# Kernel optimization log

Hardware: AMD Instinct MI355X
Metric: run time of the kernel (lower is better)

The kernel has to match this reference:

```python
import jax, jax.numpy as jnp
import numpy as np

NUM_HEADS = 12

def _attn(q, k, v, scale):
    # q,k,v: [..., L, hd]; softmax attention over L (key axis)
    s = jnp.einsum('...qd,...kd->...qk', q, k) * scale
    a = jax.nn.softmax(s, axis=-1)
    return jnp.einsum('...qk,...kd->...qd', a, v)

def setup_inputs() -> dict:
    key = jax.random.key(0)
    k1, k2, k3 = jax.random.split(key, 3)
    B, N, C, D = 8, 256, 16, 768
    x = jax.random.normal(k1, (B, N, C, D), dtype=jnp.float32)
    w_qkv = jax.random.normal(k2, (D, 6 * D), dtype=jnp.float32) * (D ** -0.5)
    w_proj = jax.random.normal(k3, (D, D), dtype=jnp.float32) * (D ** -0.5)
    b_proj = jnp.zeros((D,), dtype=jnp.float32)
    return {"x": x, "w_qkv": w_qkv, "w_proj": w_proj, "b_proj": b_proj}

def reference(x, w_qkv, w_proj, b_proj):
    B, N, C, D = x.shape
    H = NUM_HEADS
    hd = D // H
    scale = hd ** -0.5
    # qkv: [B,N,C,6,H,hd] -> [6,B,H,N,C,hd]
    qkv = (x @ w_qkv).reshape(B, N, C, 6, H, hd).transpose(3, 0, 4, 1, 2, 5)
    qc, kc, qs, ks, vc, vs = qkv[0], qkv[1], qkv[2], qkv[3], qkv[4], qkv[5]
    # spatial attention over N (per channel c): move to [B,H,C,N,hd]
    qs = jnp.swapaxes(qs, -2, -3)
    ks = jnp.swapaxes(ks, -2, -3)
    vs = jnp.swapaxes(vs, -2, -3)
    xs = _attn(qs, ks, vs, scale)          # [B,H,C,N,hd]
    xs = jnp.swapaxes(xs, -2, -3)          # [B,H,N,C,hd]
    # channel attention over C (per token n)
    xc = _attn(qc, kc, vc, scale)          # [B,H,N,C,hd]
    out = xs * xc                           # elementwise combine (fused path)
    # matches torch: x.transpose(1,2).reshape(B,N,C,D)
    out = out.transpose(0, 2, 1, 3, 4).reshape(B, N, C, D)
    return out @ w_proj + b_proj
```

## Files before the change

kernel.cpp:

```cpp
#include <hip/hip_runtime.h>

typedef _Float16 f16;
typedef f16  f16x8 __attribute__((ext_vector_type(8)));
typedef float f32x4 __attribute__((ext_vector_type(4)));

#define S3 3145728LL

__device__ __forceinline__ f32x4 mm(f16x8 a, f16x8 b, f32x4 c) {
  return __builtin_amdgcn_mfma_f32_16x16x32_f16(a, b, c, 0, 0, 0);
}
__device__ __forceinline__ void BAR() { asm volatile("s_barrier" ::: "memory"); }

__device__ __forceinline__ int esw(int t, int col) {
  return t * 128 + ((((col >> 3) ^ ((t ^ (t >> 3)) & 7)) << 3) | (col & 7));
}

__global__ void cvt_T_kernel(const float* __restrict__ in, f16* __restrict__ out,
                             int R, int Cc) {
  __shared__ float tile[32][33];
  int tc = blockIdx.x, tr = blockIdx.y;
  int lr = threadIdx.x & 31, lw = threadIdx.x >> 5;
  int c0 = tc * 32, r0 = tr * 32;
#pragma unroll
  for (int i = 0; i < 4; i++)
    tile[lw + 8 * i][lr] = in[(size_t)(r0 + lw + 8 * i) * Cc + c0 + lr];
  __syncthreads();
#pragma unroll
  for (int i = 0; i < 4; i++)
    out[(size_t)(c0 + lw + 8 * i) * R + r0 + lr] = (f16)tile[lr][lw + 8 * i];
}

__global__ void cvt_x_kernel(const float* __restrict__ in, f16* __restrict__ out) {
  size_t i = ((size_t)blockIdx.x * 256 + threadIdx.x) * 8;
  f32x4 a = __builtin_nontemporal_load((const f32x4*)(in + i));
  f32x4 b = __builtin_nontemporal_load((const f32x4*)(in + i + 4));
  f16x8 o;
#pragma unroll
  for (int j = 0; j < 4; j++) { o[j] = (f16)a[j]; o[4 + j] = (f16)b[j]; }
  *(f16x8*)(out + i) = o;
}

#define QST_A(c, q, kt) __builtin_amdgcn_global_load_lds( \
    (const __attribute__((address_space(1))) void*)(aSrc + (size_t)(q) * 24576 + (size_t)(kt) * 64), \
    (__attribute__((address_space(3))) void*)((char*)lds + (c) * 32768 + (q) * 1024 * 4 + wave * 1024), 16, 0, 0)
#define QST_B(c, q, kt) __builtin_amdgcn_global_load_lds( \
    (const __attribute__((address_space(1))) void*)(bSrc + (size_t)(q) * 24576 + (size_t)(kt) * 64), \
    (__attribute__((address_space(3))) void*)((char*)lds + 16384 + (c) * 32768 + (q) * 1024 * 4 + wave * 1024), 16, 0, 0)

__global__ __launch_bounds__(256, 2) void gemm_qkvT(
    const f16* __restrict__ A, const f16* __restrict__ Bt,
    f16* __restrict__ area, long long cstr_) {
  __shared__ f16 lds[32768];
  size_t cstr = (size_t)cstr_;
  int id  = blockIdx.x;
  int cpx = gridDim.x >> 3;
  int id2 = (id & 7) * cpx + (id >> 3);
  int sr = id2 / 288, rr = id2 % 288;
  int bm = sr * 8 + (rr & 7), bn = rr >> 3;

  int tid = threadIdx.x;
  int wave = tid >> 6, lane = tid & 63;
  int l16 = lane & 15, lq = lane >> 4;
  int wr = wave >> 1, wc = wave & 1;
  int l7 = l16 & 7;
  int cb0 = ((lq) ^ l7) << 4;
  int cb1 = ((4 + lq) ^ l7) << 4;

  const f16* aSrc = A  + (size_t)(bm * 128 + (tid >> 3)) * 768 +
                    (((tid & 7) ^ ((tid >> 3) & 7)) << 3);
  const f16* bSrc = Bt + (size_t)(bn * 128 + (tid >> 3)) * 768 +
                    (((tid & 7) ^ ((tid >> 3) & 7)) << 3);

  f32x4 zz = {0.f, 0.f, 0.f, 0.f};
  f32x4 acc[4][4];
#pragma unroll
  for (int m = 0; m < 4; m++)
#pragma unroll
    for (int n = 0; n < 4; n++) acc[m][n] = zz;

#pragma unroll
  for (int q = 0; q < 4; q++) { QST_A(0, q, 0); }
#pragma unroll
  for (int q = 0; q < 4; q++) { QST_B(0, q, 0); }
#pragma unroll
  for (int q = 0; q < 4; q++) { QST_A(1, q, 1); }
#pragma unroll
  for (int q = 0; q < 4; q++) { QST_B(1, q, 1); }
  asm volatile("s_waitcnt vmcnt(8)" ::: "memory");
  BAR();

  f16x8 af[4][2], bf[4][2];
#pragma unroll 2
  for (int t = 0; t < 12; ++t) {
    int c = t & 1;
    const char* ab = (const char*)lds + c * 32768;
    const char* bb = ab + 16384;
    int rA = wr * 64 + l16;
    int rB = wc * 64 + l16;
#pragma unroll
    for (int mf = 0; mf < 4; mf++) {
      af[mf][0] = *(const f16x8*)(ab + (rA + mf * 16) * 128 + cb0);
      af[mf][1] = *(const f16x8*)(ab + (rA + mf * 16) * 128 + cb1);
    }
#pragma unroll
    for (int nf = 0; nf < 4; nf++) {
      bf[nf][0] = *(const f16x8*)(bb + (rB + nf * 16) * 128 + cb0);
      bf[nf][1] = *(const f16x8*)(bb + (rB + nf * 16) * 128 + cb1);
    }
    asm volatile("s_waitcnt lgkmcnt(0)" ::: "memory");
    BAR();
    if (t < 10) {
#pragma unroll
      for (int q = 0; q < 4; q++) { QST_A(c, q, t + 2); }
#pragma unroll
      for (int q = 0; q < 4; q++) { QST_B(c, q, t + 2); }
    }
    __builtin_amdgcn_s_setprio(1);
#pragma unroll
    for (int ks = 0; ks < 2; ks++)
#pragma unroll
      for (int mf = 0; mf < 4; mf++)
#pragma unroll
        for (int nf = 0; nf < 4; nf++)
          acc[mf][nf] = mm(af[mf][ks], bf[nf][ks], acc[mf][nf]);
    __builtin_amdgcn_s_setprio(0);
    if (t < 10) asm volatile("s_waitcnt vmcnt(8)" ::: "memory");
    else        asm volatile("s_waitcnt vmcnt(0)" ::: "memory");
    BAR();
  }

  int s  = bn / 6;
  int h0 = (bn % 6) * 2;
  size_t comp;
  if (s == 0) comp = 0; else if (s == 1) comp = 1; else if (s == 2) comp = 3;
  else if (s == 3) comp = 4; else if (s == 4) comp = 2; else comp = 5;
  int g = (bm * 128) >> 12;
  size_t base = comp * cstr + (size_t)g * S3;
  int n0 = (bm & 31) * 8;

  __syncthreads();
#pragma unroll
  for (int mi = 0; mi < 4; mi++)
#pragma unroll
    for (int ni = 0; ni < 4; ni++)
#pragma unroll
      for (int r = 0; r < 4; r++) {
        int t = wr * 64 + mi * 16 + lq * 4 + r;
        int col = wc * 64 + ni * 16 + l16;
        lds[esw(t, col)] = (f16)acc[mi][ni][r];
      }
  __syncthreads();

  if (s < 2) {
#pragma unroll
    for (int i = 0; i < 4; i++) {
      int u = wave * 4 + i;
      int hl = u >> 3, j16 = u & 7;
#pragma unroll
      for (int half = 0; half < 2; half++) {
        int e0 = half * 512 + lane * 8;
        int cc = e0 >> 6, d0 = e0 & 63;
        f16x8 v = *(const f16x8*)&lds[esw(j16 * 16 + cc, hl * 64 + d0)];
        __builtin_nontemporal_store(v, (f16x8*)&area[base +
            (size_t)(h0 + hl) * 262144 + (size_t)(n0 + j16) * 1024 + e0]);
      }
    }
  } else if (s < 4) {
#pragma unroll
    for (int i = 0; i < 8; i++) {
      int u = wave * 8 + i;
      int hl = u >> 4, cc = u & 15;
      int e = lane * 8;
      int nl = e >> 6, d0 = e & 63;
      f16x8 v = *(const f16x8*)&lds[esw(nl * 16 + cc, hl * 64 + d0)];
      __builtin_nontemporal_store(v, (f16x8*)&area[base +
          (size_t)((h0 + hl) * 16 + cc) * 16384 + (size_t)n0 * 64 + e]);
    }
  } else if (s == 4) {
#pragma unroll
    for (int i = 0; i < 4; i++) {
      int u = wave * 4 + i;
      int hl = u >> 3, j8 = u & 7;
#pragma unroll
      for (int half = 0; half < 2; half++) {
        int e0 = half * 512 + lane * 8;
        int d0 = e0 >> 4, cb = e0 & 15;
        f16x8 v;
#pragma unroll
        for (int j = 0; j < 8; j++)
          v[j] = lds[esw(j8 * 16 + cb + j, hl * 64 + d0)];
        __builtin_nontemporal_store(v, (f16x8*)&area[base +
            (size_t)((h0 + hl) * 256 + n0 + j8) * 1024 + e0]);
      }
    }
  } else {
#pragma unroll
    for (int i = 0; i < 8; i++) {
      int u = wave * 8 + i;
      int hl = u >> 4, cc = u & 15;
      int e = lane * 8;
      int d0 = e >> 3;
      f16x8 v;
#pragma unroll
      for (int j = 0; j < 8; j++)
        v[j] = lds[esw(j * 16 + cc, hl * 64 + d0)];
      __builtin_nontemporal_store(v, (f16x8*)&area[base +
          ((size_t)((h0 + hl) * 16 + cc) * 32 + (bm & 31)) * 512 + e]);
    }
  }
}

#define STG_A(c, q, kt) __builtin_amdgcn_global_load_lds( \
    (const __attribute__((address_space(1))) void*)(aSrc + (size_t)(q) * 49152 + (size_t)(kt) * 64), \
    (__attribute__((address_space(3))) void*)(lds + (c) * 32768 + (q) * 4096 + wave * 512), 16, 0, 0)
#define STG_B(c, q, kt) __builtin_amdgcn_global_load_lds( \
    (const __attribute__((address_space(1))) void*)(bSrc + (size_t)(q) * 49152 + (size_t)(kt) * 64), \
    (__attribute__((address_space(3))) void*)(lds + 16384 + (c) * 32768 + (q) * 4096 + wave * 512), 16, 0, 0)

__global__ __launch_bounds__(512, 2) void gemm_proj8(
    const f16* __restrict__ A, const f16* __restrict__ Bt,
    const float* __restrict__ bias, float* __restrict__ Cout) {
  __shared__ f16 lds[65536];
  int id  = blockIdx.x;
  int cpx = gridDim.x >> 3;
  int id2 = (id & 7) * cpx + (id >> 3);
  int sr = id2 / 24, rr = id2 % 24;
  int bm = sr * 8 + (rr & 7), bn = rr >> 3;

  int tid = threadIdx.x;
  int wave = tid >> 6, lane = tid & 63;
  int l16 = lane & 15, lq = lane >> 4;
  int wr = wave >> 2, wc = wave & 3;
  int sx  = (l16 & 7) << 4;
  int cb0 = (lq * 16) ^ sx;
  int cb1 = (64 + lq * 16) ^ sx;

  int scol = ((tid & 7) ^ ((tid >> 3) & 7)) << 3;
  const f16* aSrc = A  + (size_t)(bm * 256 + (tid >> 3)) * 768 + scol;
  const f16* bSrc = Bt + (size_t)(bn * 256 + (tid >> 3)) * 768 + scol;

  f32x4 zz = {0.f, 0.f, 0.f, 0.f};
  f32x4 acc[8][4];
#pragma unroll
  for (int m = 0; m < 8; m++)
#pragma unroll
    for (int n = 0; n < 4; n++) acc[m][n] = zz;

  STG_A(0, 0, 0); STG_A(0, 1, 0); STG_A(0, 2, 0); STG_A(0, 3, 0);
  STG_B(0, 0, 0); STG_B(0, 1, 0); STG_B(0, 2, 0); STG_B(0, 3, 0);
  STG_A(1, 1, 1); STG_A(1, 3, 1);
  STG_B(1, 0, 1); STG_B(1, 1, 1);
  asm volatile("s_waitcnt vmcnt(4)" ::: "memory");
  BAR();

  f16x8 af[4][2], ag[4][2], bf[2][2], bg[2][2];
#pragma unroll 2
  for (int t = 0; t < 12; ++t) {
    int c = t & 1, nb = c ^ 1;
    const char* ab = (const char*)lds + c * 65536;
    const char* bb = ab + 32768;
    int rA = wr * 128 + l16;
    int rB = wc * 64 + l16;
#pragma unroll
    for (int mf = 0; mf < 4; mf++) {
      af[mf][0] = *(const f16x8*)(ab + (rA + mf * 16) * 128 + cb0);
      af[mf][1] = *(const f16x8*)(ab + (rA + mf * 16) * 128 + cb1);
    }
#pragma unroll
    for (int nf = 0; nf < 2; nf++) {
      bf[nf][0] = *(const f16x8*)(bb + (rB + nf * 16) * 128 + cb0);
      bf[nf][1] = *(const f16x8*)(bb + (rB + nf * 16) * 128 + cb1);
      bg[nf][0] = *(const f16x8*)(bb + (rB + 32 + nf * 16) * 128 + cb0);
      bg[nf][1] = *(const f16x8*)(bb + (rB + 32 + nf * 16) * 128 + cb1);
    }
    if (t < 11) {
      STG_B(nb, 2, t + 1); STG_B(nb, 3, t + 1);
      STG_A(nb, 0, t + 1); STG_A(nb, 2, t + 1);
    }
    BAR();
    __builtin_amdgcn_s_setprio(1);
#pragma unroll
    for (int ks = 0; ks < 2; ks++)
#pragma unroll
      for (int mf = 0; mf < 4; mf++)
#pragma unroll
        for (int nf = 0; nf < 2; nf++) {
          acc[mf][nf]     = mm(af[mf][ks], bf[nf][ks], acc[mf][nf]);
          acc[mf][2 + nf] = mm(af[mf][ks], bg[nf][ks], acc[mf][2 + nf]);
        }
    __builtin_amdgcn_s_setprio(0);
    BAR();
#pragma unroll
    for (int mf = 0; mf < 4; mf++) {
      ag[mf][0] = *(const f16x8*)(ab + (rA + 64 + mf * 16) * 128 + cb0);
      ag[mf][1] = *(const f16x8*)(ab + (rA + 64 + mf * 16) * 128 + cb1);
    }
    if (t < 10) {
      STG_A(c, 1, t + 2); STG_A(c, 3, t + 2);
      STG_B(c, 0, t + 2); STG_B(c, 1, t + 2);
    }
    BAR();
    __builtin_amdgcn_s_setprio(1);
#pragma unroll
    for (int ks = 0; ks < 2; ks++)
#pragma unroll
      for (int mf = 0; mf < 4; mf++)
#pragma unroll
        for (int nf = 0; nf < 2; nf++) {
          acc[4 + mf][nf]     = mm(ag[mf][ks], bf[nf][ks], acc[4 + mf][nf]);
          acc[4 + mf][2 + nf] = mm(ag[mf][ks], bg[nf][ks], acc[4 + mf][2 + nf]);
        }
    __builtin_amdgcn_s_setprio(0);
    if (t < 10) asm volatile("s_waitcnt vmcnt(4)" ::: "memory");
    else        asm volatile("s_waitcnt vmcnt(0)" ::: "memory");
    BAR();
  }

#pragma unroll
  for (int ni = 0; ni < 4; ni++) {
    int col = bn * 256 + wc * 64 + ni * 16 + l16;
    float bb = bias[col];
#pragma unroll
    for (int mi = 0; mi < 8; mi++) {
#pragma unroll
      for (int r = 0; r < 4; r++) {
        int row = bm * 256 + wr * 128 + (mi >> 2) * 64 + (mi & 3) * 16 + lq * 4 + r;
        __builtin_nontemporal_store(acc[mi][ni][r] + bb,
                                    &Cout[(size_t)row * 768 + col]);
      }
    }
  }
}

__global__ __launch_bounds__(512) void attn_spat_kernel(f16* __restrict__ area,
                                                        long long cstr_) {
  size_t cstr = (size_t)cstr_;
  int blk = blockIdx.x;
  int g = blk / 192, rem = blk % 192;
  int h = rem >> 4, c = rem & 15;
  size_t goff = (size_t)g * S3;
  const f16* qs = area + 3 * cstr + goff + (size_t)((h * 16 + c) * 256) * 64;
  const f16* ks = area + 4 * cstr + goff + (size_t)((h * 16 + c) * 256) * 64;
  const f16* vsb = area + 5 * cstr + goff + (size_t)(h * 16 + c) * 16384;
  f16* xs = area + 6 * cstr + goff + (size_t)((h * 16 + c) * 256) * 64;

  int wave = threadIdx.x >> 6, lane = threadIdx.x & 63;
  int l16 = lane & 15, lq = lane >> 4;
  __shared__ f16 plds[8][32][40];

  f32x4 zz = {0.f, 0.f, 0.f, 0.f};
  f16x8 aq[2][2];
#pragma unroll
  for (int m = 0; m < 2; m++)
#pragma unroll
    for (int kd = 0; kd < 2; kd++)
      aq[m][kd] = *(const f16x8*)&qs[(size_t)(wave * 32 + m * 16 + l16) * 64 + kd * 32 + lq * 8];

  f32x4 o[2][4];
  float mrow[2][4], lrow[2][4];
#pragma unroll
  for (int m = 0; m < 2; m++) {
#pragma unroll
    for (int n = 0; n < 4; n++) o[m][n] = zz;
#pragma unroll
    for (int r = 0; r < 4; r++) { mrow[m][r] = -1e30f; lrow[m][r] = 0.f; }
  }

  for (int kc = 0; kc < 8; kc++) {
    int k0 = kc * 32;
    f16x8 bk00 = *(const f16x8*)&ks[(size_t)(k0 + l16) * 64 + lq * 8];
    f16x8 bk01 = *(const f16x8*)&ks[(size_t)(k0 + l16) * 64 + 32 + lq * 8];
    f16x8 bk10 = *(const f16x8*)&ks[(size_t)(k0 + 16 + l16) * 64 + lq * 8];
    f16x8 bk11 = *(const f16x8*)&ks[(size_t)(k0 + 16 + l16) * 64 + 32 + lq * 8];
    f32x4 st[2][2];
#pragma unroll
    for (int m = 0; m < 2; m++) {
      st[m][0] = mm(aq[m][1], bk01, mm(aq[m][0], bk00, zz));
      st[m][1] = mm(aq[m][1], bk11, mm(aq[m][0], bk10, zz));
    }
#pragma unroll
    for (int m = 0; m < 2; m++) {
#pragma unroll
      for (int r = 0; r < 4; r++) {
        float s0 = st[m][0][r] * 0.125f, s1 = st[m][1][r] * 0.125f;
        float t = fmaxf(s0, s1);
        t = fmaxf(t, __shfl_xor(t, 1));
        t = fmaxf(t, __shfl_xor(t, 2));
        t = fmaxf(t, __shfl_xor(t, 4));
        t = fmaxf(t, __shfl_xor(t, 8));
        float mold = mrow[m][r];
        float mnew = fmaxf(mold, t);
        float fac  = __expf(mold - mnew);
        mrow[m][r] = mnew;
        float p0 = __expf(s0 - mnew), p1 = __expf(s1 - mnew);
        lrow[m][r] = lrow[m][r] * fac + p0 + p1;
        o[m][0][r] *= fac; o[m][1][r] *= fac; o[m][2][r] *= fac; o[m][3][r] *= fac;
        int prow = m * 16 + lq * 4 + r;
        plds[wave][prow][l16]      = (f16)p0;
        plds[wave][prow][16 + l16] = (f16)p1;
      }
    }
    f16x8 ap0 = *(const f16x8*)&plds[wave][l16][lq * 8];
    f16x8 ap1 = *(const f16x8*)&plds[wave][16 + l16][lq * 8];
#pragma unroll
    for (int n = 0; n < 4; n++) {
      f16x8 bv = *(const f16x8*)&vsb[((k0 >> 3) + lq) * 512 + (n * 16 + l16) * 8];
      o[0][n] = mm(ap0, bv, o[0][n]);
      o[1][n] = mm(ap1, bv, o[1][n]);
    }
  }
#pragma unroll
  for (int m = 0; m < 2; m++)
#pragma unroll
    for (int r = 0; r < 4; r++) {
      float l = lrow[m][r];
      l += __shfl_xor(l, 1);
      l += __shfl_xor(l, 2);
      l += __shfl_xor(l, 4);
      l += __shfl_xor(l, 8);
      lrow[m][r] = 1.0f / l;
    }
#pragma unroll
  for (int m = 0; m < 2; m++)
#pragma unroll
    for (int n = 0; n < 4; n++)
#pragma unroll
      for (int r = 0; r < 4; r++) {
        int row = wave * 32 + m * 16 + lq * 4 + r;
        xs[(size_t)row * 64 + n * 16 + l16] = (f16)(o[m][n][r] * lrow[m][r]);
      }
}

__global__ __launch_bounds__(256) void attn_chan_kernel(f16* __restrict__ area,
                                                        long long cstr_) {
  size_t cstr = (size_t)cstr_;
  int blk = blockIdx.x;
  int g = blk >> 8, n = blk & 255;
  size_t goff = (size_t)g * S3;
  int wave = threadIdx.x >> 6, lane = threadIdx.x & 63;
  int l16 = lane & 15, lq = lane >> 4;
  __shared__ f16 plds[4][16][40];
  if (lane < 16) {
#pragma unroll
    for (int j = 0; j < 16; j++) plds[wave][lane][16 + j] = (f16)0.f;
  }
  const f16* xs = area + 6 * cstr + goff;
  f16* prod = area + 7 * cstr + goff;
  f32x4 zz = {0.f, 0.f, 0.f, 0.f};
  for (int hi = 0; hi < 3; hi++) {
    int h = wave + hi * 4;
    const f16* q = area + 0 * cstr + goff + (size_t)((h * 256 + n) * 16) * 64;
    const f16* k = area + 1 * cstr + goff + (size_t)((h * 256 + n) * 16) * 64;
    const f16* v = area + 2 * cstr + goff + (size_t)((h * 256 + n) * 64) * 16;
    f16x8 a0 = *(const f16x8*)&q[l16 * 64 + lq * 8];
    f16x8 a1 = *(const f16x8*)&q[l16 * 64 + 32 + lq * 8];
    f16x8 b0 = *(const f16x8*)&k[l16 * 64 + lq * 8];
    f16x8 b1 = *(const f16x8*)&k[l16 * 64 + 32 + lq * 8];
    f32x4 s = mm(a1, b1, mm(a0, b0, zz));
    float p[4];
#pragma unroll
    for (int r = 0; r < 4; r++) {
      float t = s[r] * 0.125f;
      float mx = t;
      mx = fmaxf(mx, __shfl_xor(mx, 1));
      mx = fmaxf(mx, __shfl_xor(mx, 2));
      mx = fmaxf(mx, __shfl_xor(mx, 4));
      mx = fmaxf(mx, __shfl_xor(mx, 8));
      float e = __expf(t - mx);
      float sum = e;
      sum += __shfl_xor(sum, 1);
      sum += __shfl_xor(sum, 2);
      sum += __shfl_xor(sum, 4);
      sum += __shfl_xor(sum, 8);
      p[r] = e / sum;
    }
#pragma unroll
    for (int r = 0; r < 4; r++)
      plds[wave][lq * 4 + r][l16] = (f16)p[r];
    f16x8 ap = *(const f16x8*)&plds[wave][l16][lq * 8];
#pragma unroll
    for (int nt = 0; nt < 4; nt++) {
      f16x8 bv = *(const f16x8*)&v[(nt * 16 + l16) * 16 + lq * 8];
      f32x4 o = mm(ap, bv, zz);
#pragma unroll
      for (int r = 0; r < 4; r++) {
        int cq = lq * 4 + r, d = nt * 16 + l16;
        float xsv = (float)xs[(size_t)((h * 16 + cq) * 256 + n) * 64 + d];
        prod[(size_t)n * 12288 + h * 1024 + cq * 64 + d] = (f16)(o[r] * xsv);
      }
    }
  }
}

extern "C" void kernel_launch(void* const* d_in, const int* in_sizes, int n_in,
                              void* d_out, int out_size, void* d_ws, size_t ws_size,
                              hipStream_t stream) {
  const float* x      = (const float*)d_in[0];
  const float* w_qkv  = (const float*)d_in[1];
  const float* w_proj = (const float*)d_in[2];
  const float* b_proj = (const float*)d_in[3];
  float* out = (float*)d_out;
  f16* ws = (f16*)d_ws;

  const size_t W16T = 4608ull * 768;
  const size_t WPT  = 768ull * 768;
  f16* w16t = ws;
  f16* wpt  = ws + W16T;
  f16* area = wpt + WPT;

  int G = 8;
  while (G > 1 && (W16T + WPT + 8ull * G * S3) * 2 > ws_size) G >>= 1;
  int nch = 8 / G;
  long long cstr = (long long)G * S3;
  f16* x16 = area + 7 * (size_t)cstr;

  cvt_T_kernel<<<dim3(144, 24), 256, 0, stream>>>(w_qkv, w16t, 768, 4608);
  cvt_T_kernel<<<dim3(24, 24), 256, 0, stream>>>(w_proj, wpt, 768, 768);

  for (int ch = 0; ch < nch; ch++) {
    size_t b0 = (size_t)ch * G;
    cvt_x_kernel<<<G * 1536, 256, 0, stream>>>(x + b0 * S3, x16);
    gemm_qkvT<<<G * 1152, 256, 0, stream>>>(x16, w16t, area, cstr);
    attn_spat_kernel<<<G * 192, 512, 0, stream>>>(area, cstr);
    attn_chan_kernel<<<G * 256, 256, 0, stream>>>(area, cstr);
    gemm_proj8<<<G * 48, 512, 0, stream>>>(area + 7 * (size_t)cstr, wpt, b_proj,
                                           out + b0 * S3);
  }
}
```

Measured before the change: 573.0 us.

## Store spatial attention output token-major and stage channel-kernel I/O through LDS

The spatial attention kernel now writes its output into a swizzled LDS tile and then emits 16-byte nontemporal stores in a token-major layout ([n][h][c][d]). The channel kernel can then read each token's 12288-element xs slice contiguously with global_load_lds, and its product is staged in LDS before being written out with vectorised nontemporal stores. Previously both kernels did strided 2-byte scalar global accesses. The change adds about 32KB of LDS in the spatial kernel and 48KB in the channel kernel, which may reduce occupancy.

```diff
diff --git a/kernel.cpp b/kernel.cpp
--- a/kernel.cpp
+++ b/kernel.cpp
@@ -13,6 +13,9 @@
 
 __device__ __forceinline__ int esw(int t, int col) {
   return t * 128 + ((((col >> 3) ^ ((t ^ (t >> 3)) & 7)) << 3) | (col & 7));
+}
+__device__ __forceinline__ int oesw(int t, int col) {
+  return t * 64 + ((((col >> 3) ^ (t & 7)) << 3) | (col & 7));
 }
 
 __global__ void cvt_T_kernel(const float* __restrict__ in, f16* __restrict__ out,
@@ -342,11 +345,13 @@
   const f16* qs = area + 3 * cstr + goff + (size_t)((h * 16 + c) * 256) * 64;
   const f16* ks = area + 4 * cstr + goff + (size_t)((h * 16 + c) * 256) * 64;
   const f16* vsb = area + 5 * cstr + goff + (size_t)(h * 16 + c) * 16384;
-  f16* xs = area + 6 * cstr + goff + (size_t)((h * 16 + c) * 256) * 64;
-
-  int wave = threadIdx.x >> 6, lane = threadIdx.x & 63;
+  f16* xsn = area + 6 * cstr + goff;
+
+  int tid = threadIdx.x;
+  int wave = tid >> 6, lane = tid & 63;
   int l16 = lane & 15, lq = lane >> 4;
   __shared__ f16 plds[8][32][40];
+  __shared__ f16 osm[16384];
 
   f32x4 zz = {0.f, 0.f, 0.f, 0.f};
   f16x8 aq[2][2];
@@ -427,8 +432,17 @@
 #pragma unroll
       for (int r = 0; r < 4; r++) {
         int row = wave * 32 + m * 16 + lq * 4 + r;
-        xs[(size_t)row * 64 + n * 16 + l16] = (f16)(o[m][n][r] * lrow[m][r]);
-      }
+        osm[oesw(row, n * 16 + l16)] = (f16)(o[m][n][r] * lrow[m][r]);
+      }
+  __syncthreads();
+  size_t hc64 = (size_t)(h * 16 + c) * 64;
+#pragma unroll
+  for (int i = 0; i < 4; i++) {
+    int row = i * 64 + (tid >> 3);
+    int dp  = (tid & 7) * 8;
+    f16x8 v = *(const f16x8*)&osm[oesw(row, dp)];
+    __builtin_nontemporal_store(v, (f16x8*)&xsn[(size_t)row * 12288 + hc64 + dp]);
+  }
 }
 
 __global__ __launch_bounds__(256) void attn_chan_kernel(f16* __restrict__ area,
@@ -437,15 +451,28 @@
   int blk = blockIdx.x;
   int g = blk >> 8, n = blk & 255;
   size_t goff = (size_t)g * S3;
-  int wave = threadIdx.x >> 6, lane = threadIdx.x & 63;
+  int tid = threadIdx.x;
+  int wave = tid >> 6, lane = tid & 63;
   int l16 = lane & 15, lq = lane >> 4;
+  __shared__ f16 xsl[12288];
+  __shared__ f16 prl[12288];
   __shared__ f16 plds[4][16][40];
+
+  const f16* xsn = area + 6 * cstr + goff + (size_t)n * 12288;
+#pragma unroll
+  for (int i = 0; i < 6; i++) {
+    int seg = wave * 6 + i;
+    __builtin_amdgcn_global_load_lds(
+        (const __attribute__((address_space(1))) void*)(xsn + seg * 512 + lane * 8),
+        (__attribute__((address_space(3))) void*)((char*)xsl + seg * 1024), 16, 0, 0);
+  }
   if (lane < 16) {
 #pragma unroll
     for (int j = 0; j < 16; j++) plds[wave][lane][16 + j] = (f16)0.f;
   }
-  const f16* xs = area + 6 * cstr + goff;
-  f16* prod = area + 7 * cstr + goff;
+  asm volatile("s_waitcnt vmcnt(0)" ::: "memory");
+  __syncthreads();
+
   f32x4 zz = {0.f, 0.f, 0.f, 0.f};
   for (int hi = 0; hi < 3; hi++) {
     int h = wave + hi * 4;
@@ -485,10 +512,18 @@
 #pragma unroll
       for (int r = 0; r < 4; r++) {
         int cq = lq * 4 + r, d = nt * 16 + l16;
-        float xsv = (float)xs[(size_t)((h * 16 + cq) * 256 + n) * 64 + d];
-        prod[(size_t)n * 12288 + h * 1024 + cq * 64 + d] = (f16)(o[r] * xsv);
-      }
-    }
+        int idx = h * 1024 + cq * 64 + d;
+        float xsv = (float)xsl[idx];
+        prl[idx] = (f16)(o[r] * xsv);
+      }
+    }
+  }
+  __syncthreads();
+  f16* prod = area + 7 * cstr + goff + (size_t)n * 12288;
+#pragma unroll
+  for (int i = 0; i < 6; i++) {
+    f16x8 v = *(const f16x8*)&prl[i * 2048 + tid * 8];
+    __builtin_nontemporal_store(v, (f16x8*)&prod[i * 2048 + tid * 8]);
   }
 }
 
```

Result: faster. 544.1 us (-5.0%).
